# Optimization experiments

Hardware: AMD Instinct MI355X
Metric: run time of the kernel (lower is better)

Reference implementation:

```python
import jax, jax.numpy as jnp
import numpy as np

B, S, D, H, F, E, K = 2, 2048, 1024, 16, 4096, 8, 2
DH = D // H
EPS = 1e-6  # RMSNorm eps (torch nn.RMSNorm default ~ fp32 machine eps; 1e-6 used here)


def _rmsnorm(x, w):
    return x * jax.lax.rsqrt(jnp.mean(x * x, axis=-1, keepdims=True) + EPS) * w


def setup_inputs() -> dict:
    key = jax.random.key(0)
    ks = jax.random.split(key, 16)
    std = 0.02
    return {
        "x": jax.random.normal(ks[0], (B, S, D), jnp.float32),
        "norm1_w": jnp.ones((D,), jnp.float32),
        "norm2_w": jnp.ones((D,), jnp.float32),
        "w_qkv": jax.random.normal(ks[1], (D, 3 * D), jnp.float32) * std,
        "b_qkv": jnp.zeros((3 * D,), jnp.float32),
        "w_o": jax.random.normal(ks[2], (D, D), jnp.float32) * std,
        "b_o": jnp.zeros((D,), jnp.float32),
        "router_w": jax.random.normal(ks[3], (D, E), jnp.float32) * std,
        "router_b": jnp.zeros((E,), jnp.float32),
        "w1": jax.random.normal(ks[4], (E, D, F), jnp.float32) * std,
        "b1": jnp.zeros((E, F), jnp.float32),
        "w2": jax.random.normal(ks[5], (E, F, D), jnp.float32) * std,
        "b2": jnp.zeros((E, D), jnp.float32),
    }


def reference(x, norm1_w, norm2_w, w_qkv, b_qkv, w_o, b_o,
              router_w, router_b, w1, b1, w2, b2):
    # ---- pre-norm causal multi-head attention ----
    h = _rmsnorm(x, norm1_w)
    qkv = h @ w_qkv + b_qkv                                  # [B,S,3D]
    q, k, v = jnp.split(qkv, 3, axis=-1)
    q = q.reshape(B, S, H, DH).transpose(0, 2, 1, 3)         # [B,H,S,DH]
    k = k.reshape(B, S, H, DH).transpose(0, 2, 1, 3)
    v = v.reshape(B, S, H, DH).transpose(0, 2, 1, 3)
    scores = jnp.einsum('bhqd,bhkd->bhqk', q, k) / jnp.sqrt(jnp.asarray(DH, x.dtype))
    causal = jnp.tril(jnp.ones((S, S), bool))
    scores = jnp.where(causal, scores, jnp.asarray(-1e9, x.dtype))
    attn = jax.nn.softmax(scores, axis=-1)
    ao = jnp.einsum('bhqk,bhkd->bhqd', attn, v).transpose(0, 2, 1, 3).reshape(B, S, D)
    x = x + (ao @ w_o + b_o)

    # ---- pre-norm top-k MoE feed-forward ----
    h2 = _rmsnorm(x, norm2_w)
    t = h2.reshape(-1, D)                                    # [T,D], T=B*S
    logits = t @ router_w + router_b                         # [T,E]
    probs = jax.nn.softmax(logits, axis=-1)
    topv, topi = jax.lax.top_k(probs, K)                     # [T,K]
    gates_k = topv / jnp.sum(topv, axis=-1, keepdims=True)   # renormalized top-k gates
    oh = jax.nn.one_hot(topi, E, dtype=x.dtype)              # [T,K,E]
    gates = jnp.einsum('tke,tk->te', oh, gates_k)            # dense gates, zero off top-k

    out = jnp.zeros_like(t)
    for e in range(E):                                       # fixed small expert loop
        he = jax.nn.gelu(t @ w1[e] + b1[e], approximate=False)
        ye = he @ w2[e] + b2[e]
        out = out + gates[:, e:e + 1] * ye

    # load-balancing aux loss: E * sum_e f_e * P_e
    f = jnp.mean(jnp.sum(oh, axis=1), axis=0)                # fraction routed to each expert
    P = jnp.mean(probs, axis=0)                              # mean router prob per expert
    aux_loss = jnp.asarray(E, x.dtype) * jnp.sum(f * P)

    x = x + out.reshape(B, S, D)
    return (x, aux_loss)
```

## Files before the change

kernel.cpp:

```cpp
#include <hip/hip_runtime.h>
#include <math.h>

#define TB 2
#define TS 2048
#define TD 1024
#define TH 16
#define TDH 64
#define TF 4096
#define TE 8
#define TT 4096
#define PSTR (TB*TH*TS*TDH)

typedef __attribute__((ext_vector_type(8))) __bf16 bf16x8;
typedef __attribute__((ext_vector_type(4))) float f32x4;
typedef __attribute__((ext_vector_type(8))) short short8;
typedef __attribute__((ext_vector_type(4))) unsigned short ushort4v;
typedef __attribute__((ext_vector_type(4))) float fvec4;

__device__ inline unsigned short f2bf(float f) {
  union { float f; unsigned int u; } v; v.f = f;
  unsigned int u = v.u;
  unsigned int r = (u + 0x7FFFu + ((u >> 16) & 1u)) >> 16;
  return (unsigned short)r;
}
__device__ inline float bf2f(unsigned short h) {
  union { unsigned int u; float f; } v; v.u = ((unsigned int)h) << 16; return v.f;
}
__device__ inline void split2(float x, unsigned short& h, unsigned short& m) {
  h = f2bf(x);
  m = f2bf(x - bf2f(h));
}

__device__ inline f32x4 mfma_bf16(short8 a, short8 b, f32x4 c) {
  return __builtin_amdgcn_mfma_f32_16x16x32_bf16(
      __builtin_bit_cast(bf16x8, a), __builtin_bit_cast(bf16x8, b), c, 0, 0, 0);
}

__device__ inline void gload16(const void* g, void* l) {
  __builtin_amdgcn_global_load_lds(
      (const __attribute__((address_space(1))) void*)g,
      (__attribute__((address_space(3))) void*)l, 16, 0, 0);
}

__global__ __launch_bounds__(256)
void tcvt_kernel(const float* __restrict__ In, unsigned short* __restrict__ Out,
                 int R, int C) {
  __shared__ float tile[32][33];
  In  += (size_t)blockIdx.z * R * C;
  Out += (size_t)blockIdx.z * R * C;
  int c0 = blockIdx.x * 32, r0 = blockIdx.y * 32;
  int tx = threadIdx.x & 31, ty = threadIdx.x >> 5;
#pragma unroll
  for (int i = 0; i < 4; ++i)
    tile[ty + 8*i][tx] = In[(size_t)(r0 + ty + 8*i) * C + c0 + tx];
  __syncthreads();
#pragma unroll
  for (int i = 0; i < 4; ++i)
    Out[(size_t)(c0 + ty + 8*i) * R + r0 + tx] = f2bf(tile[tx][ty + 8*i]);
}

__global__ __launch_bounds__(256)
void tcvt_split_kernel(const float* __restrict__ In,
                       unsigned short* __restrict__ O0,
                       unsigned short* __restrict__ O1, int R, int C) {
  __shared__ float tile[32][33];
  int c0 = blockIdx.x * 32, r0 = blockIdx.y * 32;
  int tx = threadIdx.x & 31, ty = threadIdx.x >> 5;
#pragma unroll
  for (int i = 0; i < 4; ++i)
    tile[ty + 8*i][tx] = In[(size_t)(r0 + ty + 8*i) * C + c0 + tx];
  __syncthreads();
#pragma unroll
  for (int i = 0; i < 4; ++i) {
    float v = tile[tx][ty + 8*i];
    unsigned short h, m; split2(v, h, m);
    size_t idx = (size_t)(c0 + ty + 8*i) * R + r0 + tx;
    O0[idx] = h; O1[idx] = m;
  }
}

__global__ __launch_bounds__(256)
void rmsnorm_kernel(const float* __restrict__ X, const float* __restrict__ W,
                    unsigned short* __restrict__ O) {
  int row = blockIdx.x;
  int tid = threadIdx.x;
  int lane = tid & 63, wave = tid >> 6;
  const float* xr = X + (size_t)row * TD;
  fvec4 v = *(const fvec4*)(xr + tid * 4);
  float ss = v[0]*v[0] + v[1]*v[1] + v[2]*v[2] + v[3]*v[3];
#pragma unroll
  for (int msk = 1; msk < 64; msk <<= 1) ss += __shfl_xor(ss, msk);
  __shared__ float red[4];
  if (lane == 0) red[wave] = ss;
  __syncthreads();
  ss = red[0] + red[1] + red[2] + red[3];
  float rs = rsqrtf(ss * (1.0f / TD) + 1e-6f);
  fvec4 wv = *(const fvec4*)(W + tid * 4);
  ushort4v o;
#pragma unroll
  for (int j = 0; j < 4; ++j) o[j] = f2bf(v[j] * rs * wv[j]);
  *(ushort4v*)(O + (size_t)row * TD + tid * 4) = o;
}

__global__ __launch_bounds__(256)
void rmsnorm_split_kernel(const float* __restrict__ X, const float* __restrict__ W,
                          unsigned short* __restrict__ O0,
                          unsigned short* __restrict__ O1) {
  int row = blockIdx.x;
  int tid = threadIdx.x;
  int lane = tid & 63, wave = tid >> 6;
  const float* xr = X + (size_t)row * TD;
  fvec4 v = *(const fvec4*)(xr + tid * 4);
  float ss = v[0]*v[0] + v[1]*v[1] + v[2]*v[2] + v[3]*v[3];
#pragma unroll
  for (int msk = 1; msk < 64; msk <<= 1) ss += __shfl_xor(ss, msk);
  __shared__ float red[4];
  if (lane == 0) red[wave] = ss;
  __syncthreads();
  ss = red[0] + red[1] + red[2] + red[3];
  float rs = rsqrtf(ss * (1.0f / TD) + 1e-6f);
  fvec4 wv = *(const fvec4*)(W + tid * 4);
  ushort4v o0, o1;
#pragma unroll
  for (int j = 0; j < 4; ++j) {
    unsigned short h, m; split2(v[j] * rs * wv[j], h, m);
    o0[j] = h; o1[j] = m;
  }
  size_t idx = (size_t)row * TD + tid * 4;
  *(ushort4v*)(O0 + idx) = o0;
  *(ushort4v*)(O1 + idx) = o1;
}

template<int MODE>
__global__ __launch_bounds__(256)
void gemm2(const unsigned short* __restrict__ A0,
           const unsigned short* __restrict__ A1,
           const unsigned short* __restrict__ B0,
           const unsigned short* __restrict__ B1,
           const float* __restrict__ bias, int Kd,
           float* __restrict__ outF, const float* __restrict__ resid,
           unsigned short* __restrict__ S0,
           unsigned short* __restrict__ S1) {
  __shared__ __align__(16) unsigned short As0[2][4096], As1[2][4096];
  __shared__ __align__(16) unsigned short Bs0[2][4096], Bs1[2][4096];
  const int tid = threadIdx.x;
  const int lane = tid & 63;
  const int w = tid >> 6;
  const int wr = w >> 1, wc = w & 1;
  const int g = lane >> 4;
  const int l15 = lane & 15;
  const int m0 = blockIdx.y * 128;
  const int n0 = blockIdx.x * 128;

  const int c_swz = (lane & 3) ^ ((lane >> 3) & 3);
  const unsigned short *a0p[2], *a1p[2], *b0p[2], *b1p[2];
  int ldsrow[2];
#pragma unroll
  for (int j = 0; j < 2; ++j) {
    int r16 = w * 2 + j;
    int r = r16 * 16 + (lane >> 2);
    a0p[j] = A0 + (size_t)(m0 + r) * Kd + c_swz * 8;
    a1p[j] = A1 + (size_t)(m0 + r) * Kd + c_swz * 8;
    b0p[j] = B0 + (size_t)(n0 + r) * Kd + c_swz * 8;
    b1p[j] = B1 + (size_t)(n0 + r) * Kd + c_swz * 8;
    ldsrow[j] = r16 * 512;
  }

#define G2_STAGE(p, koff)                              \
  {                                                    \
    _Pragma("unroll")                                  \
    for (int j = 0; j < 2; ++j) {                      \
      gload16(a0p[j] + (koff), &As0[p][ldsrow[j]]);    \
      gload16(a1p[j] + (koff), &As1[p][ldsrow[j]]);    \
      gload16(b0p[j] + (koff), &Bs0[p][ldsrow[j]]);    \
      gload16(b1p[j] + (koff), &Bs1[p][ldsrow[j]]);    \
    }                                                  \
  }

  f32x4 acc[4][4] = {};
  const int nt = Kd >> 5;

  G2_STAGE(0, 0);
  for (int t = 0; t < nt; ++t) {
    const int p = t & 1;
    if (t + 1 < nt) {
      G2_STAGE(p ^ 1, (t + 1) * 32);
      asm volatile("s_waitcnt vmcnt(8)" ::: "memory");
    } else {
      asm volatile("s_waitcnt vmcnt(0)" ::: "memory");
    }
    __builtin_amdgcn_s_barrier();

    short8 a0f[4], a1f[4], b0f[4], b1f[4];
#pragma unroll
    for (int mi = 0; mi < 4; ++mi) {
      int row = wr * 64 + mi * 16 + l15;
      int off = (row * 64 + g * 16) ^ (((row >> 1) & 3) << 4);
      a0f[mi] = *(const short8*)((const char*)As0[p] + off);
      a1f[mi] = *(const short8*)((const char*)As1[p] + off);
    }
#pragma unroll
    for (int ni = 0; ni < 4; ++ni) {
      int row = wc * 64 + ni * 16 + l15;
      int off = (row * 64 + g * 16) ^ (((row >> 1) & 3) << 4);
      b0f[ni] = *(const short8*)((const char*)Bs0[p] + off);
      b1f[ni] = *(const short8*)((const char*)Bs1[p] + off);
    }
#pragma unroll
    for (int mi = 0; mi < 4; ++mi)
#pragma unroll
      for (int ni = 0; ni < 4; ++ni) {
        f32x4 tacc = acc[mi][ni];
        tacc = mfma_bf16(a0f[mi], b0f[ni], tacc);
        tacc = mfma_bf16(a0f[mi], b1f[ni], tacc);
        tacc = mfma_bf16(a1f[mi], b0f[ni], tacc);
        acc[mi][ni] = tacc;
      }
    __builtin_amdgcn_s_barrier();
  }
#undef G2_STAGE

#pragma unroll
  for (int mi = 0; mi < 4; ++mi) {
#pragma unroll
    for (int ni = 0; ni < 4; ++ni) {
      int n = n0 + wc * 64 + ni * 16 + l15;
      float bv = bias[n];
      if (MODE == 0) {
        int part = n >> 10, d = n & 1023, hh = d >> 6, dh = d & 63;
        int s0r = m0 + wr * 64 + mi * 16 + g * 4;
        int b = s0r >> 11, s_ = s0r & 2047;
        int bh = b * TH + hh;
        if (part < 2) {
          size_t base = (size_t)part * PSTR + (size_t)bh * (TS * TDH) + (size_t)s_ * TDH + dh;
#pragma unroll
          for (int r = 0; r < 4; ++r) {
            unsigned short h, m; split2(acc[mi][ni][r] + bv, h, m);
            size_t idx = base + (size_t)r * TDH;
            S0[idx] = h; S1[idx] = m;
          }
        } else {
          ushort4v o0, o1;
#pragma unroll
          for (int r = 0; r < 4; ++r) {
            unsigned short h, m; split2(acc[mi][ni][r] + bv, h, m);
            o0[r] = h; o1[r] = m;
          }
          size_t idx = 2 * (size_t)PSTR + (size_t)bh * (TS * TDH) + (size_t)dh * TS + s_;
          *(ushort4v*)(S0 + idx) = o0;
          *(ushort4v*)(S1 + idx) = o1;
        }
      } else {
#pragma unroll
        for (int r = 0; r < 4; ++r) {
          int m = m0 + wr * 64 + mi * 16 + g * 4 + r;
          size_t idx = (size_t)m * TD + n;
          outF[idx] = acc[mi][ni][r] + bv + resid[idx];
        }
      }
    }
  }
}

__global__ __launch_bounds__(512, 4)
void attn2_kernel(const unsigned short* __restrict__ S0,
                  const unsigned short* __restrict__ S1,
                  unsigned short* __restrict__ A0,
                  unsigned short* __restrict__ A1) {
  __shared__ __align__(16) char Kt0[8192], Kt1[8192];
  __shared__ __align__(16) char Vt0[8192], Vt1[8192];
  __shared__ __align__(16) char Pt0[16384], Pt1[16384];

  const int tid = threadIdx.x;
  const int lane = tid & 63;
  const int wave = tid >> 6;
  const int g = lane >> 4, l15 = lane & 15;

  const int bh = blockIdx.y;
  const int b = bh >> 4, hh = bh & 15;

  const size_t qbase = (size_t)bh * TS * TDH;
  const size_t kbase = (size_t)PSTR + qbase;
  const size_t vbase = 2 * (size_t)PSTR + qbase;

  for (int half = 0; half < 2; ++half) {
    const int qtb = half ? (15 - (int)blockIdx.x) : (int)blockIdx.x;
    const int qlo = qtb * 128 + wave * 16;

    short8 aq0[2], aq1[2];
#pragma unroll
    for (int c = 0; c < 2; ++c) {
      size_t qo = qbase + (size_t)(qlo + l15) * TDH + c * 32 + g * 8;
      aq0[c] = *(const short8*)(S0 + qo);
      aq1[c] = *(const short8*)(S1 + qo);
    }

    f32x4 accv[4] = {};
    float m_[4] = {-1e30f, -1e30f, -1e30f, -1e30f};
    float l_[4] = {0.f, 0.f, 0.f, 0.f};

    const int ktmax = 2 * qtb + 1;
    for (int kt = 0; kt <= ktmax; ++kt) {
      __syncthreads();
      {
        int row = tid >> 3, ch = tid & 7;
        int off = (row * 128 + ch * 16) ^ ((row & 7) << 4);
        size_t kg = kbase + (size_t)(kt * 64 + row) * TDH + ch * 8;
        *(short8*)(Kt0 + off) = *(const short8*)(S0 + kg);
        *(short8*)(Kt1 + off) = *(const short8*)(S1 + kg);
        size_t vg = vbase + (size_t)row * TS + kt * 64 + ch * 8;
        *(short8*)(Vt0 + off) = *(const short8*)(S0 + vg);
        *(short8*)(Vt1 + off) = *(const short8*)(S1 + vg);
      }
      __syncthreads();

      if (kt * 64 > qlo + 15) continue;
      const bool needmask = (kt * 64 + 63 > qlo);

      f32x4 sf[4] = {};
#pragma unroll
      for (int kb = 0; kb < 4; ++kb) {
#pragma unroll
        for (int c = 0; c < 2; ++c) {
          int krow = kb * 16 + l15;
          int off = (krow * 128 + (c * 32 + g * 8) * 2) ^ ((krow & 7) << 4);
          short8 bk0 = *(const short8*)(Kt0 + off);
          short8 bk1 = *(const short8*)(Kt1 + off);
          f32x4 t = sf[kb];
          t = mfma_bf16(aq0[c], bk0, t);
          t = mfma_bf16(aq0[c], bk1, t);
          t = mfma_bf16(aq1[c], bk0, t);
          sf[kb] = t;
        }
      }

      float pv[4][4];
#pragma unroll
      for (int r = 0; r < 4; ++r) {
        float s0 = sf[0][r] * 0.125f, s1 = sf[1][r] * 0.125f;
        float s2 = sf[2][r] * 0.125f, s3 = sf[3][r] * 0.125f;
        if (needmask) {
          int qg = qlo + g * 4 + r;
          int k0g = kt * 64 + l15;
          if (k0g      > qg) s0 = -1e30f;
          if (k0g + 16 > qg) s1 = -1e30f;
          if (k0g + 32 > qg) s2 = -1e30f;
          if (k0g + 48 > qg) s3 = -1e30f;
        }
        float mx = fmaxf(fmaxf(s0, s1), fmaxf(s2, s3));
#pragma unroll
        for (int msk = 1; msk < 16; msk <<= 1) mx = fmaxf(mx, __shfl_xor(mx, msk));
        float nm = fmaxf(m_[r], mx);
        float sc = __expf(m_[r] - nm);
        float p0 = __expf(s0 - nm), p1 = __expf(s1 - nm);
        float p2 = __expf(s2 - nm), p3 = __expf(s3 - nm);
        float rs = p0 + p1 + p2 + p3;
#pragma unroll
        for (int msk = 1; msk < 16; msk <<= 1) rs += __shfl_xor(rs, msk);
        m_[r] = nm;
        l_[r] = l_[r] * sc + rs;
#pragma unroll
        for (int dhb = 0; dhb < 4; ++dhb) accv[dhb][r] *= sc;
        pv[0][r] = p0; pv[1][r] = p1; pv[2][r] = p2; pv[3][r] = p3;
      }

      char* P0 = Pt0 + wave * 2048;
      char* P1 = Pt1 + wave * 2048;
#pragma unroll
      for (int kb = 0; kb < 4; ++kb) {
#pragma unroll
        for (int r = 0; r < 4; ++r) {
          int prow = g * 4 + r;
          int key = kb * 16 + l15;
          int off = (prow * 128 + key * 2) ^ ((prow & 7) << 4);
          unsigned short h, m; split2(pv[kb][r], h, m);
          *(unsigned short*)(P0 + off) = h;
          *(unsigned short*)(P1 + off) = m;
        }
      }
      short8 pa0[2], pa1[2];
#pragma unroll
      for (int c = 0; c < 2; ++c) {
        int off = (l15 * 128 + (c * 32 + g * 8) * 2) ^ ((l15 & 7) << 4);
        pa0[c] = *(const short8*)(P0 + off);
        pa1[c] = *(const short8*)(P1 + off);
      }
#pragma unroll
      for (int dhb = 0; dhb < 4; ++dhb) {
#pragma unroll
        for (int c = 0; c < 2; ++c) {
          int dh = dhb * 16 + l15;
          int off = (dh * 128 + (c * 32 + g * 8) * 2) ^ ((dh & 7) << 4);
          short8 bv0 = *(const short8*)(Vt0 + off);
          short8 bv1 = *(const short8*)(Vt1 + off);
          f32x4 t = accv[dhb];
          t = mfma_bf16(pa0[c], bv0, t);
          t = mfma_bf16(pa0[c], bv1, t);
          t = mfma_bf16(pa1[c], bv0, t);
          accv[dhb] = t;
        }
      }
    }

#pragma unroll
    for (int dhb = 0; dhb < 4; ++dhb) {
#pragma unroll
      for (int r = 0; r < 4; ++r) {
        int srow = qlo + g * 4 + r;
        int col = hh * 64 + dhb * 16 + l15;
        unsigned short h, m; split2(accv[dhb][r] / l_[r], h, m);
        size_t idx = ((size_t)(b * TS + srow)) * TD + col;
        A0[idx] = h; A1[idx] = m;
      }
    }
  }
}

template<int MODE>
__global__ __launch_bounds__(256)
void gemm_bt(const unsigned short* __restrict__ A,
             const unsigned short* __restrict__ Bt,
             const float* __restrict__ bias,
             int N, int Kd,
             float* __restrict__ ysl,
             unsigned short* __restrict__ outH,
             const int* __restrict__ seg_off,
             const int* __restrict__ seg_cnt,
             const int* __restrict__ token_perm,
             const float* __restrict__ gate_perm) {
  __shared__ __align__(16) unsigned short As[2][4096];
  __shared__ __align__(16) unsigned short Bs[2][4096];
  __shared__ int tok[128];

  const int tid = threadIdx.x;
  const int lane = tid & 63;
  const int w = tid >> 6;
  const int wr = w >> 1, wc = w & 1;
  const int g = lane >> 4;
  const int l15 = lane & 15;

  const int e = blockIdx.z;
  const int m0 = blockIdx.y * 128;
  const int n0 = blockIdx.x * 128;
  const int off = seg_off[e];
  const int Mrows = seg_cnt[e];
  if (m0 >= Mrows) return;
  Bt += (size_t)e * N * Kd;
  bias += (size_t)e * N;
  if (tid < 128) {
    int r = m0 + tid;
    int rc = (r < Mrows) ? r : (Mrows - 1);
    tok[tid] = (MODE == 2) ? token_perm[off + rc] : (off + rc);
  }
  __syncthreads();

  const int c_swz = (lane & 3) ^ ((lane >> 3) & 3);
  const unsigned short* aptr[2];
  const unsigned short* bptr[2];
  int ldsrow[2];
#pragma unroll
  for (int j = 0; j < 2; ++j) {
    int r16 = w * 2 + j;
    int r = r16 * 16 + (lane >> 2);
    aptr[j] = A + (size_t)tok[r] * Kd + c_swz * 8;
    bptr[j] = Bt + (size_t)(n0 + r) * Kd + c_swz * 8;
    ldsrow[j] = r16 * 512;
  }

#define GB_STAGE(p, koff)                           \
  {                                                 \
    _Pragma("unroll")                               \
    for (int j = 0; j < 2; ++j) {                   \
      gload16(aptr[j] + (koff), &As[p][ldsrow[j]]); \
      gload16(bptr[j] + (koff), &Bs[p][ldsrow[j]]); \
    }                                               \
  }

  f32x4 acc[4][4] = {};
  const int nt = Kd >> 5;

  GB_STAGE(0, 0);
  for (int t = 0; t < nt; ++t) {
    const int p = t & 1;
    if (t + 1 < nt) {
      GB_STAGE(p ^ 1, (t + 1) * 32);
      asm volatile("s_waitcnt vmcnt(4)" ::: "memory");
    } else {
      asm volatile("s_waitcnt vmcnt(0)" ::: "memory");
    }
    __builtin_amdgcn_s_barrier();

    short8 af[4], bfr[4];
#pragma unroll
    for (int mi = 0; mi < 4; ++mi) {
      int row = wr * 64 + mi * 16 + l15;
      int o2 = (row * 64 + g * 16) ^ (((row >> 1) & 3) << 4);
      af[mi] = *(const short8*)((const char*)As[p] + o2);
    }
#pragma unroll
    for (int ni = 0; ni < 4; ++ni) {
      int row = wc * 64 + ni * 16 + l15;
      int o2 = (row * 64 + g * 16) ^ (((row >> 1) & 3) << 4);
      bfr[ni] = *(const short8*)((const char*)Bs[p] + o2);
    }
#pragma unroll
    for (int mi = 0; mi < 4; ++mi)
#pragma unroll
      for (int ni = 0; ni < 4; ++ni)
        acc[mi][ni] = mfma_bf16(af[mi], bfr[ni], acc[mi][ni]);
    __builtin_amdgcn_s_barrier();
  }
#undef GB_STAGE

#pragma unroll
  for (int mi = 0; mi < 4; ++mi) {
#pragma unroll
    for (int ni = 0; ni < 4; ++ni) {
      int n = n0 + wc * 64 + ni * 16 + l15;
      float bv = bias[n];
#pragma unroll
      for (int r = 0; r < 4; ++r) {
        int mloc = m0 + wr * 64 + mi * 16 + g * 4 + r;
        if (mloc >= Mrows) continue;
        float val = acc[mi][ni][r] + bv;
        if (MODE == 2) {
          float ge = 0.5f * val * (1.0f + erff(val * 0.70710678118654752f));
          outH[(size_t)(off + mloc) * TF + n] = f2bf(ge);
        } else {
          float gv = gate_perm[off + mloc];
          ysl[(size_t)(off + mloc) * TD + n] = gv * val;
        }
      }
    }
  }
}

__global__ __launch_bounds__(256)
void moe_reduce_kernel(const float* __restrict__ ys, const int* __restrict__ tslot,
                       float* __restrict__ out) {
  int t = blockIdx.x;
  int d = threadIdx.x * 4;
  fvec4 a = *(const fvec4*)(ys + (size_t)tslot[t * 2] * TD + d);
  fvec4 b = *(const fvec4*)(ys + (size_t)tslot[t * 2 + 1] * TD + d);
  float* o = out + (size_t)t * TD + d;
  fvec4 c = *(const fvec4*)o;
#pragma unroll
  for (int j = 0; j < 4; ++j) c[j] += a[j] + b[j];
  *(fvec4*)o = c;
}

__global__ __launch_bounds__(256)
void router_kernel(const float* __restrict__ X1, const float* __restrict__ N2W,
                   const float* __restrict__ RW, const float* __restrict__ RB,
                   int* __restrict__ top_e, float* __restrict__ top_g,
                   int* __restrict__ counts, float* __restrict__ p_sum) {
  __shared__ float s_psum[TE];
  __shared__ int s_cnt[TE];
  if (threadIdx.x < TE) { s_psum[threadIdx.x] = 0.f; s_cnt[threadIdx.x] = 0; }
  __syncthreads();
  int lane = threadIdx.x & 63, wave = threadIdx.x >> 6;
  for (int it = 0; it < 16; ++it) {
    int t = (blockIdx.x * 4 + wave) * 16 + it;
    const float* xr = X1 + (size_t)t * TD;
    float vals[16]; float ss = 0.f;
#pragma unroll
    for (int i = 0; i < 16; ++i) { float xv = xr[i * 64 + lane]; vals[i] = xv; ss += xv * xv; }
#pragma unroll
    for (int msk = 1; msk < 64; msk <<= 1) ss += __shfl_xor(ss, msk);
    float rs = rsqrtf(ss * (1.0f / TD) + 1e-6f);
    float acc[TE] = {};
#pragma unroll
    for (int i = 0; i < 16; ++i) {
      int d = i * 64 + lane;
      float nv = vals[i] * rs * N2W[d];
      const float* rwp = RW + (size_t)d * TE;
#pragma unroll
      for (int e2 = 0; e2 < TE; ++e2) acc[e2] += nv * rwp[e2];
    }
#pragma unroll
    for (int msk = 1; msk < 64; msk <<= 1)
#pragma unroll
      for (int e2 = 0; e2 < TE; ++e2) acc[e2] += __shfl_xor(acc[e2], msk);
    if (lane == 0) {
      float lg[TE]; float mx = -1e30f;
      for (int e2 = 0; e2 < TE; ++e2) { lg[e2] = acc[e2] + RB[e2]; mx = fmaxf(mx, lg[e2]); }
      float sum = 0.f, pe[TE];
      for (int e2 = 0; e2 < TE; ++e2) { pe[e2] = expf(lg[e2] - mx); sum += pe[e2]; }
      float inv = 1.0f / sum;
      for (int e2 = 0; e2 < TE; ++e2) atomicAdd(&s_psum[e2], pe[e2] * inv);
      int i1 = 0;
      for (int e2 = 1; e2 < TE; ++e2) if (lg[e2] > lg[i1]) i1 = e2;
      int i2 = (i1 == 0) ? 1 : 0;
      for (int e2 = 0; e2 < TE; ++e2) if (e2 != i1 && lg[e2] > lg[i2]) i2 = e2;
      float g1 = pe[i1], g2 = pe[i2], gs = g1 + g2;
      top_e[t * 2] = i1; top_e[t * 2 + 1] = i2;
      top_g[t * 2] = g1 / gs; top_g[t * 2 + 1] = g2 / gs;
      atomicAdd(&s_cnt[i1], 1); atomicAdd(&s_cnt[i2], 1);
    }
  }
  __syncthreads();
  if (threadIdx.x < TE) {
    atomicAdd(&p_sum[threadIdx.x], s_psum[threadIdx.x]);
    atomicAdd(&counts[threadIdx.x], s_cnt[threadIdx.x]);
  }
}

__global__ void zero_meta_kernel(int* counts, float* p_sum) {
  int t = threadIdx.x;
  if (t < TE) { counts[t] = 0; p_sum[t] = 0.f; }
}

__global__ void offsets_kernel(const int* counts, int* offs, int* cursor) {
  if (threadIdx.x == 0) {
    int o = 0;
    for (int e2 = 0; e2 < TE; ++e2) { offs[e2] = o; o += counts[e2]; }
  }
  if (threadIdx.x < TE) cursor[threadIdx.x] = 0;
}

__global__ __launch_bounds__(256)
void fill_kernel(const int* __restrict__ top_e, const float* __restrict__ top_g,
                 const int* __restrict__ offs, int* __restrict__ cursor,
                 int* __restrict__ token_perm, float* __restrict__ gate_perm,
                 int* __restrict__ tslot) {
  __shared__ int s_cnt[TE], s_base[TE];
  if (threadIdx.x < TE) s_cnt[threadIdx.x] = 0;
  __syncthreads();
  int t = blockIdx.x * 256 + threadIdx.x;
  int e0 = top_e[t * 2], e1 = top_e[t * 2 + 1];
  int r0 = atomicAdd(&s_cnt[e0], 1);
  int r1 = atomicAdd(&s_cnt[e1], 1);
  __syncthreads();
  if (threadIdx.x < TE)
    s_base[threadIdx.x] = atomicAdd(&cursor[threadIdx.x], s_cnt[threadIdx.x]);
  __syncthreads();
  int p0 = offs[e0] + s_base[e0] + r0;
  int p1 = offs[e1] + s_base[e1] + r1;
  token_perm[p0] = t; gate_perm[p0] = top_g[t * 2];
  token_perm[p1] = t; gate_perm[p1] = top_g[t * 2 + 1];
  tslot[t * 2] = p0; tslot[t * 2 + 1] = p1;
}

__global__ void aux_kernel(const int* counts, const float* p_sum, float* outv) {
  if (threadIdx.x == 0) {
    float a = 0.f;
    for (int e2 = 0; e2 < TE; ++e2)
      a += ((float)counts[e2] / (float)TT) * (p_sum[e2] / (float)TT);
    outv[0] = (float)TE * a;
  }
}

extern "C" void kernel_launch(void* const* d_in, const int* in_sizes, int n_in,
                              void* d_out, int out_size, void* d_ws, size_t ws_size,
                              hipStream_t stream) {
  const float* x     = (const float*)d_in[0];
  const float* n1w   = (const float*)d_in[1];
  const float* n2w   = (const float*)d_in[2];
  const float* w_qkv = (const float*)d_in[3];
  const float* b_qkv = (const float*)d_in[4];
  const float* w_o   = (const float*)d_in[5];
  const float* b_o   = (const float*)d_in[6];
  const float* rw    = (const float*)d_in[7];
  const float* rb    = (const float*)d_in[8];
  const float* w1    = (const float*)d_in[9];
  const float* b1    = (const float*)d_in[10];
  const float* w2    = (const float*)d_in[11];
  const float* b2    = (const float*)d_in[12];
  float* out = (float*)d_out;
  char* ws = (char*)d_ws;

  size_t o = 0;
  auto give = [&](size_t bytes) -> char* {
    char* p = ws + o;
    o += (bytes + 255) & ~(size_t)255;
    return p;
  };
  unsigned short* w1T = (unsigned short*)give(8ull * 4096 * 1024 * 2);
  unsigned short* w2T = (unsigned short*)give(8ull * 1024 * 4096 * 2);
  unsigned short* wo0 = (unsigned short*)give(1024ull * 1024 * 2);
  unsigned short* wo1 = (unsigned short*)give(1024ull * 1024 * 2);
  unsigned short* h2  = (unsigned short*)give((size_t)TT * TD * 2);
  int*   counts = (int*)give(TE * 4);
  int*   cursor = (int*)give(TE * 4);
  int*   offs   = (int*)give(TE * 4);
  float* psum   = (float*)give(TE * 4);
  int*   top_e  = (int*)give(2ull * TT * 4);
  float* top_g  = (float*)give(2ull * TT * 4);
  int*   tperm  = (int*)give(2ull * TT * 4);
  float* gperm  = (float*)give(2ull * TT * 4);
  int*   tslot  = (int*)give(2ull * TT * 4);
  unsigned short* wq0 = (unsigned short*)give(3072ull * 1024 * 2);
  unsigned short* wq1 = (unsigned short*)give(3072ull * 1024 * 2);
  float* ys = (float*)give(2ull * TT * TD * 4);
  char* poolB = give(2ull * TT * TD * 2);
  unsigned short* h10 = (unsigned short*)poolB;
  unsigned short* h11 = (unsigned short*)(poolB + (size_t)TT * TD * 2);
  unsigned short* ao0 = h10; unsigned short* ao1 = h11;
  char* poolC = give(64ull * 1024 * 1024);
  unsigned short* qs0 = (unsigned short*)poolC;
  unsigned short* qs1 = (unsigned short*)(poolC + 3ull * PSTR * 2);
  unsigned short* he  = (unsigned short*)poolC;

  tcvt_split_kernel<<<dim3(96, 32, 1), 256, 0, stream>>>(w_qkv, wq0, wq1, 1024, 3072);
  tcvt_split_kernel<<<dim3(32, 32, 1), 256, 0, stream>>>(w_o, wo0, wo1, 1024, 1024);
  tcvt_kernel<<<dim3(128, 32, 8), 256, 0, stream>>>(w1, w1T, 1024, 4096);
  tcvt_kernel<<<dim3(32, 128, 8), 256, 0, stream>>>(w2, w2T, 4096, 1024);

  rmsnorm_split_kernel<<<dim3(TT), 256, 0, stream>>>(x, n1w, h10, h11);
  gemm2<0><<<dim3(24, 32, 1), 256, 0, stream>>>(
      h10, h11, wq0, wq1, b_qkv, 1024, nullptr, nullptr, qs0, qs1);
  attn2_kernel<<<dim3(8, 32, 1), 512, 0, stream>>>(qs0, qs1, ao0, ao1);
  gemm2<1><<<dim3(8, 32, 1), 256, 0, stream>>>(
      ao0, ao1, wo0, wo1, b_o, 1024, out, x, nullptr, nullptr);

  rmsnorm_kernel<<<dim3(TT), 256, 0, stream>>>(out, n2w, h2);
  zero_meta_kernel<<<dim3(1), 64, 0, stream>>>(counts, psum);
  router_kernel<<<dim3(64), 256, 0, stream>>>(out, n2w, rw, rb, top_e, top_g, counts, psum);
  offsets_kernel<<<dim3(1), 64, 0, stream>>>(counts, offs, cursor);
  fill_kernel<<<dim3(TT / 256), 256, 0, stream>>>(top_e, top_g, offs, cursor, tperm, gperm, tslot);
  gemm_bt<2><<<dim3(32, 32, 8), 256, 0, stream>>>(
      h2, w1T, b1, 4096, 1024, nullptr, he, offs, counts, tperm, gperm);
  gemm_bt<3><<<dim3(8, 32, 8), 256, 0, stream>>>(
      he, w2T, b2, 1024, 4096, ys, nullptr, offs, counts, tperm, gperm);
  moe_reduce_kernel<<<dim3(TT), 256, 0, stream>>>(ys, tslot, out);
  aux_kernel<<<dim3(1), 64, 0, stream>>>(counts, psum, out + (size_t)TT * TD);
}
```

Measured before the change: 749.4 us.

## Prefetch attention K/V tiles into registers, triple-buffer MoE GEMM, raise MFMA priority

The attention kernel now loads the next K/V tile into registers while the current tile is computed, and writes it to shared memory at the start of the next iteration. This hides global-load latency behind the MFMA work. The MoE expert GEMM moves from double to triple buffering of its shared-memory stages, keeping two global loads in flight. s_setprio is raised around the MFMA blocks in all three GEMM and attention loops so waves issuing matrix ops get scheduling priority. In exchange, shared-memory use and register pressure go up, which can lower occupancy.

```diff
diff --git a/kernel.cpp b/kernel.cpp
--- a/kernel.cpp
+++ b/kernel.cpp
@@ -206,6 +206,7 @@
       b0f[ni] = *(const short8*)((const char*)Bs0[p] + off);
       b1f[ni] = *(const short8*)((const char*)Bs1[p] + off);
     }
+    __builtin_amdgcn_s_setprio(1);
 #pragma unroll
     for (int mi = 0; mi < 4; ++mi)
 #pragma unroll
@@ -216,6 +217,7 @@
         tacc = mfma_bf16(a1f[mi], b0f[ni], tacc);
         acc[mi][ni] = tacc;
       }
+    __builtin_amdgcn_s_setprio(0);
     __builtin_amdgcn_s_barrier();
   }
 #undef G2_STAGE
@@ -283,6 +285,9 @@
   const size_t kbase = (size_t)PSTR + qbase;
   const size_t vbase = 2 * (size_t)PSTR + qbase;
 
+  const int srow_ = tid >> 3, sch = tid & 7;
+  const int soff = (srow_ * 128 + sch * 16) ^ ((srow_ & 7) << 4);
+
   for (int half = 0; half < 2; ++half) {
     const int qtb = half ? (15 - (int)blockIdx.x) : (int)blockIdx.x;
     const int qlo = qtb * 128 + wave * 16;
@@ -300,17 +305,31 @@
     float l_[4] = {0.f, 0.f, 0.f, 0.f};
 
     const int ktmax = 2 * qtb + 1;
+
+    short8 nk0, nk1, nv0, nv1;
+    {
+      size_t kg = kbase + (size_t)srow_ * TDH + sch * 8;
+      nk0 = *(const short8*)(S0 + kg);
+      nk1 = *(const short8*)(S1 + kg);
+      size_t vg = vbase + (size_t)srow_ * TS + sch * 8;
+      nv0 = *(const short8*)(S0 + vg);
+      nv1 = *(const short8*)(S1 + vg);
+    }
+
     for (int kt = 0; kt <= ktmax; ++kt) {
       __syncthreads();
+      *(short8*)(Kt0 + soff) = nk0;
+      *(short8*)(Kt1 + soff) = nk1;
+      *(short8*)(Vt0 + soff) = nv0;
+      *(short8*)(Vt1 + soff) = nv1;
       {
-        int row = tid >> 3, ch = tid & 7;
-        int off = (row * 128 + ch * 16) ^ ((row & 7) << 4);
-        size_t kg = kbase + (size_t)(kt * 64 + row) * TDH + ch * 8;
-        *(short8*)(Kt0 + off) = *(const short8*)(S0 + kg);
-        *(short8*)(Kt1 + off) = *(const short8*)(S1 + kg);
-        size_t vg = vbase + (size_t)row * TS + kt * 64 + ch * 8;
-        *(short8*)(Vt0 + off) = *(const short8*)(S0 + vg);
-        *(short8*)(Vt1 + off) = *(const short8*)(S1 + vg);
+        int ktn = (kt + 1 <= ktmax) ? kt + 1 : ktmax;
+        size_t kg = kbase + (size_t)(ktn * 64 + srow_) * TDH + sch * 8;
+        nk0 = *(const short8*)(S0 + kg);
+        nk1 = *(const short8*)(S1 + kg);
+        size_t vg = vbase + (size_t)srow_ * TS + ktn * 64 + sch * 8;
+        nv0 = *(const short8*)(S0 + vg);
+        nv1 = *(const short8*)(S1 + vg);
       }
       __syncthreads();
 
@@ -318,6 +337,7 @@
       const bool needmask = (kt * 64 + 63 > qlo);
 
       f32x4 sf[4] = {};
+      __builtin_amdgcn_s_setprio(1);
 #pragma unroll
       for (int kb = 0; kb < 4; ++kb) {
 #pragma unroll
@@ -333,6 +353,7 @@
           sf[kb] = t;
         }
       }
+      __builtin_amdgcn_s_setprio(0);
 
       float pv[4][4];
 #pragma unroll
@@ -385,6 +406,7 @@
         pa0[c] = *(const short8*)(P0 + off);
         pa1[c] = *(const short8*)(P1 + off);
       }
+      __builtin_amdgcn_s_setprio(1);
 #pragma unroll
       for (int dhb = 0; dhb < 4; ++dhb) {
 #pragma unroll
@@ -400,6 +422,7 @@
           accv[dhb] = t;
         }
       }
+      __builtin_amdgcn_s_setprio(0);
     }
 
 #pragma unroll
@@ -428,8 +451,8 @@
              const int* __restrict__ seg_cnt,
              const int* __restrict__ token_perm,
              const float* __restrict__ gate_perm) {
-  __shared__ __align__(16) unsigned short As[2][4096];
-  __shared__ __align__(16) unsigned short Bs[2][4096];
+  __shared__ __align__(16) unsigned short As[3][4096];
+  __shared__ __align__(16) unsigned short Bs[3][4096];
   __shared__ int tok[128];
 
   const int tid = threadIdx.x;
@@ -480,10 +503,13 @@
   const int nt = Kd >> 5;
 
   GB_STAGE(0, 0);
+  GB_STAGE(1, 32);
   for (int t = 0; t < nt; ++t) {
-    const int p = t & 1;
-    if (t + 1 < nt) {
-      GB_STAGE(p ^ 1, (t + 1) * 32);
+    const int p = t % 3;
+    if (t + 2 < nt) {
+      GB_STAGE((t + 2) % 3, (t + 2) * 32);
+      asm volatile("s_waitcnt vmcnt(8)" ::: "memory");
+    } else if (t + 1 < nt) {
       asm volatile("s_waitcnt vmcnt(4)" ::: "memory");
     } else {
       asm volatile("s_waitcnt vmcnt(0)" ::: "memory");
@@ -503,11 +529,13 @@
       int o2 = (row * 64 + g * 16) ^ (((row >> 1) & 3) << 4);
       bfr[ni] = *(const short8*)((const char*)Bs[p] + o2);
     }
+    __builtin_amdgcn_s_setprio(1);
 #pragma unroll
     for (int mi = 0; mi < 4; ++mi)
 #pragma unroll
       for (int ni = 0; ni < 4; ++ni)
         acc[mi][ni] = mfma_bf16(af[mi], bfr[ni], acc[mi][ni]);
+    __builtin_amdgcn_s_setprio(0);
     __builtin_amdgcn_s_barrier();
   }
 #undef GB_STAGE
```

After: 760.7 us. About the same (+1.5%).
